# Kernel optimization log

Measured on AMD Instinct MI355X. Metric: run time of the kernel, lower is better.

## Reference

```python
import jax, jax.numpy as jnp
import numpy as np

N = 50000      # nodes
E = 800000     # edges
D_IN = 256     # state_dim
H = 128        # HIDDEN_LAYER
A = 32         # action_dim
EPS = 1e-5
NEG_SLOPE = 0.2


def setup_inputs() -> dict:
    key = jax.random.key(0)
    ks = jax.random.split(key, 16)
    s = lambda k, shape, std=0.1: jax.random.normal(k, shape, jnp.float32) * std
    return {
        "x": jax.random.normal(ks[0], (N, D_IN), jnp.float32),
        "edge_index": jax.random.randint(ks[1], (2, E), 0, N, jnp.int64),
        # GAT params
        "W": s(ks[2], (D_IN, H)),
        "a_src": s(ks[3], (H,)),
        "a_dst": s(ks[4], (H,)),
        "b_gat": jnp.zeros((H,), jnp.float32),
        # bn0
        "g0": jnp.ones((H,), jnp.float32),
        "beta0": jnp.zeros((H,), jnp.float32),
        # fc1, fc2
        "W1": s(ks[5], (H, H)),
        "b1": jnp.zeros((H,), jnp.float32),
        "W2": s(ks[6], (H, H)),
        "b2": jnp.zeros((H,), jnp.float32),
        # bn2
        "g2": jnp.ones((H,), jnp.float32),
        "beta2": jnp.zeros((H,), jnp.float32),
        # fc3
        "W3": s(ks[7], (H, A)),
        "b3": jnp.zeros((A,), jnp.float32),
    }


def _batchnorm(h, gamma, beta):
    # training-mode BN: biased batch stats over node dim
    mu = jnp.mean(h, axis=0)
    var = jnp.var(h, axis=0)
    return (h - mu) * jax.lax.rsqrt(var + EPS) * gamma + beta


def _gat(x, edge_index, W, a_src, a_dst, b_gat):
    src, dst = edge_index[0], edge_index[1]
    h = x @ W                                  # [N, H]
    e_src = h @ a_src                          # [N]
    e_dst = h @ a_dst                          # [N]
    e = jax.nn.leaky_relu(e_src[src] + e_dst[dst], NEG_SLOPE)  # [E]
    # neighbor softmax over edges grouped by destination node
    m = jax.ops.segment_max(e, dst, num_segments=N)            # [N]
    w = jnp.exp(e - m[dst])                                    # [E]
    denom = jax.ops.segment_sum(w, dst, num_segments=N)        # [N]
    alpha = w / jnp.maximum(denom, 1e-16)[dst]                 # [E]
    out = jax.ops.segment_sum(alpha[:, None] * h[src], dst, num_segments=N)
    return out + b_gat


def reference(x, edge_index, W, a_src, a_dst, b_gat, g0, beta0,
              W1, b1, W2, b2, g2, beta2, W3, b3):
    h0 = jax.nn.relu(_gat(x, edge_index, W, a_src, a_dst, b_gat))
    h0n = _batchnorm(h0, g0, beta0)
    h1 = jax.nn.relu(h0n @ W1 + b1)
    h2 = jax.nn.relu(h1 @ W2 + b2)
    h2n = _batchnorm(h2, g2, beta2)
    action = h2n @ W3 + b3
    return jax.nn.softmax(action, axis=1)
```

## Files before the change

kernel.cpp:

```cpp
#include <hip/hip_runtime.h>
#include <math.h>

#define N_NODES 50000
#define N_EDGES 800000
#define D_INPUT 256
#define HDIM 128
#define A_DIM 32
#define NEG_SLOPE 0.2f
#define BN_EPS 1e-5f
#define CAP 64
#define NB 391
#define BIN_SHIFT 7
#define BCAP 2432
#define GC_STRIDE 16
#define EPB 4096
#define FC3_TR 64
#define SROW 132

typedef short short8 __attribute__((ext_vector_type(8)));
typedef unsigned short ushort8v __attribute__((ext_vector_type(8)));
typedef unsigned short ushort4v __attribute__((ext_vector_type(4)));
typedef float float4v __attribute__((ext_vector_type(4)));

__device__ __forceinline__ unsigned short f2bf(float f) {
  unsigned u = __float_as_uint(f);
  u += 0x7FFFu + ((u >> 16) & 1u);
  return (unsigned short)(u >> 16);
}
__device__ __forceinline__ float bf2f(unsigned short b) {
  return __uint_as_float(((unsigned)b) << 16);
}

__device__ __forceinline__ float waveReduceMax(float v) {
#pragma unroll
  for (int o = 32; o >= 1; o >>= 1) v = fmaxf(v, __shfl_xor(v, o, 64));
  return v;
}
__device__ __forceinline__ float waveReduceSum(float v) {
#pragma unroll
  for (int o = 32; o >= 1; o >>= 1) v += __shfl_xor(v, o, 64);
  return v;
}

__global__ __launch_bounds__(256) void k_gemm_xw_mfma(
    const float* __restrict__ x, const unsigned short* __restrict__ Wt0,
    const float* __restrict__ a_src, const float* __restrict__ a_dst,
    unsigned short* __restrict__ hbf, float* __restrict__ esrc, float* __restrict__ edst)
{
  __shared__ short As[64][72];
  __shared__ short Bs[128][72];
  __shared__ float esred[64][2], edred[64][2];

  const int t = threadIdx.x;
  const int lane = t & 63;
  const int wv = t >> 6;
  const int rh = wv >> 1;
  const int ch = wv & 1;
  const int quad = (lane >> 4) & 3;
  const int l15 = lane & 15;
  const int row0 = blockIdx.x * 64;

  float4v acc[2][4];
#pragma unroll
  for (int i = 0; i < 2; ++i)
#pragma unroll
    for (int j = 0; j < 4; ++j) acc[i][j] = (float4v){0.f, 0.f, 0.f, 0.f};

  for (int ks = 0; ks < D_INPUT / 64; ++ks) {
    const int kk0 = ks * 64;
#pragma unroll
    for (int it = 0; it < 4; ++it) {
      int idx = it * 256 + t;
      int r = idx >> 4, c4 = idx & 15;
      int rr = row0 + r; if (rr >= N_NODES) rr = N_NODES - 1;
      float4 v = *(const float4*)(x + (size_t)rr * D_INPUT + kk0 + c4 * 4);
      ushort4v b; b.x = f2bf(v.x); b.y = f2bf(v.y); b.z = f2bf(v.z); b.w = f2bf(v.w);
      *(ushort4v*)(&As[r][c4 * 4]) = b;
    }
#pragma unroll
    for (int it = 0; it < 4; ++it) {
      int idx = it * 256 + t;
      int n = idx >> 3, c8 = idx & 7;
      *(ushort8v*)(&Bs[n][c8 * 8]) = *(const ushort8v*)(Wt0 + (size_t)n * D_INPUT + kk0 + c8 * 8);
    }
    __syncthreads();
#pragma unroll
    for (int kc = 0; kc < 2; ++kc) {
      short8 af[2], bfr[4];
#pragma unroll
      for (int rt = 0; rt < 2; ++rt)
        af[rt] = *(const short8*)(&As[rh * 32 + rt * 16 + l15][kc * 32 + quad * 8]);
#pragma unroll
      for (int nt = 0; nt < 4; ++nt)
        bfr[nt] = *(const short8*)(&Bs[ch * 64 + nt * 16 + l15][kc * 32 + quad * 8]);
#pragma unroll
      for (int rt = 0; rt < 2; ++rt)
#pragma unroll
        for (int nt = 0; nt < 4; ++nt)
          acc[rt][nt] = __builtin_amdgcn_mfma_f32_16x16x32_bf16(af[rt], bfr[nt], acc[rt][nt], 0, 0, 0);
    }
    __syncthreads();
  }

  float asv[4], adv[4];
#pragma unroll
  for (int nt = 0; nt < 4; ++nt) {
    int col = ch * 64 + nt * 16 + l15;
    asv[nt] = a_src[col]; adv[nt] = a_dst[col];
  }
#pragma unroll
  for (int rt = 0; rt < 2; ++rt) {
#pragma unroll
    for (int reg = 0; reg < 4; ++reg) {
      int rloc = rh * 32 + rt * 16 + quad * 4 + reg;
      int row = row0 + rloc;
      bool valid = (row < N_NODES);
      float ps = 0.f, pd = 0.f;
#pragma unroll
      for (int nt = 0; nt < 4; ++nt) {
        float v = acc[rt][nt][reg];
        ps += v * asv[nt]; pd += v * adv[nt];
        if (valid) hbf[(size_t)row * HDIM + ch * 64 + nt * 16 + l15] = f2bf(v);
      }
#pragma unroll
      for (int o = 8; o >= 1; o >>= 1) {
        ps += __shfl_xor(ps, o, 64);
        pd += __shfl_xor(pd, o, 64);
      }
      if (l15 == 0) { esred[rloc][ch] = ps; edred[rloc][ch] = pd; }
    }
  }
  __syncthreads();
  if (t < 64) {
    int row = row0 + t;
    if (row < N_NODES) {
      esrc[row] = esred[t][0] + esred[t][1];
      edst[row] = edred[t][0] + edred[t][1];
    }
  }
}

__global__ __launch_bounds__(256) void k_binprep(
    const int* __restrict__ srcI, const int* __restrict__ dstI,
    int* __restrict__ gcur, int* __restrict__ bbuf,
    const float* __restrict__ W, const float* __restrict__ W1,
    const float* __restrict__ W2, unsigned short* __restrict__ Wt0,
    unsigned short* __restrict__ Wt1, unsigned short* __restrict__ Wt2)
{
  const int gB = (N_EDGES + EPB - 1) / EPB;
  if (blockIdx.x >= gB) {
    int i = (blockIdx.x - gB) * 256 + threadIdx.x;
    if (i < HDIM * D_INPUT) {
      int n = i >> 8, k = i & 255;
      Wt0[i] = f2bf(W[(size_t)k * HDIM + n]);
    }
    if (i < HDIM * HDIM) {
      int n = i >> 7, k = i & 127;
      Wt1[i] = f2bf(W1[(size_t)k * HDIM + n]);
      Wt2[i] = f2bf(W2[(size_t)k * HDIM + n]);
    }
    return;
  }
  __shared__ int hist[NB];
  __shared__ int base[NB];
  const int t = threadIdx.x;
  const int e0 = blockIdx.x * EPB;
  const int e1 = min(e0 + EPB, N_EDGES);
  for (int i = t; i < NB; i += 256) hist[i] = 0;
  __syncthreads();
  for (int e = e0 + t; e < e1; e += 256)
    atomicAdd(&hist[dstI[e] >> BIN_SHIFT], 1);
  __syncthreads();
  for (int i = t; i < NB; i += 256) {
    base[i] = atomicAdd(&gcur[i * GC_STRIDE], hist[i]);
    hist[i] = 0;
  }
  __syncthreads();
  for (int e = e0 + t; e < e1; e += 256) {
    int d = dstI[e];
    int bin = d >> BIN_SHIFT;
    int r = atomicAdd(&hist[bin], 1) + base[bin];
    if (r < BCAP) bbuf[(size_t)bin * BCAP + r] = srcI[e] | ((d & 127) << 16);
  }
}

__global__ __launch_bounds__(256) void k_sc2(
    const int* __restrict__ gcur, const int* __restrict__ bbuf,
    const float* __restrict__ esrc, const float* __restrict__ edst,
    int* __restrict__ deg, int2* __restrict__ sedge)
{
  __shared__ int2 bk[128][CAP];
  __shared__ int lcur[128];
  __shared__ float ledst[128];
  const int t = threadIdx.x;
  const int bin = blockIdx.x;
  const int d0 = bin << BIN_SHIFT;
  if (t < 128) {
    lcur[t] = 0;
    int d = d0 + t;
    ledst[t] = (d < N_NODES) ? edst[d] : 0.f;
  }
  __syncthreads();
  const int cnt = min(gcur[bin * GC_STRIDE], BCAP);
  const int* seg = bbuf + (size_t)bin * BCAP;
  for (int i = t; i < cnt; i += 256) {
    int v = seg[i];
    int s = v & 0xFFFF;
    int dl = (v >> 16) & 127;
    float ev = esrc[s] + ledst[dl];
    ev = (ev > 0.f) ? ev : NEG_SLOPE * ev;
    int r = atomicAdd(&lcur[dl], 1);
    if (r < CAP) {
      int2 e2; e2.x = s; e2.y = __float_as_int(ev);
      bk[dl][r] = e2;
    }
  }
  __syncthreads();
  for (int idx = t; idx < 128 * CAP; idx += 256) {
    int dl = idx >> 6, sl = idx & 63;
    if (sl < lcur[dl])
      sedge[(size_t)(d0 + dl) * CAP + sl] = bk[dl][sl];
  }
  if (t < 128) {
    int d = d0 + t;
    if (d < N_NODES) deg[d] = min(lcur[t], CAP);
  }
}

__global__ __launch_bounds__(256) void k_agg(
    const int* __restrict__ degA, const int2* __restrict__ sedge,
    const unsigned short* __restrict__ hbf,
    const float* __restrict__ b_gat, unsigned short* __restrict__ h0)
{
  const int t = threadIdx.x;
  const int lane = t & 63;
  const int node = blockIdx.x * 4 + (t >> 6);
  const int deg = min(degA[node], CAP);

  int2 ev; ev.x = 0; ev.y = 0;
  float val = -INFINITY;
  if (lane < deg) {
    ev = sedge[(size_t)node * CAP + lane];
    val = __int_as_float(ev.y);
  }
  const float m = waveReduceMax(val);
  const float ex = (lane < deg) ? __expf(val - m) : 0.f;
  const float s = waveReduceSum(ex);
  const float al = ex * (1.0f / fmaxf(s, 1e-16f));
  const int sr = ev.x;

  float ax = 0.f, ay = 0.f;
  int j = 0;
  for (; j + 4 <= deg; j += 4) {
    float a0 = __shfl(al, j, 64),   a1 = __shfl(al, j+1, 64);
    float a2 = __shfl(al, j+2, 64), a3 = __shfl(al, j+3, 64);
    int s0 = __shfl(sr, j, 64),   s1 = __shfl(sr, j+1, 64);
    int s2 = __shfl(sr, j+2, 64), s3 = __shfl(sr, j+3, 64);
    unsigned v0 = *(const unsigned*)(hbf + (size_t)s0 * HDIM + lane * 2);
    unsigned v1 = *(const unsigned*)(hbf + (size_t)s1 * HDIM + lane * 2);
    unsigned v2 = *(const unsigned*)(hbf + (size_t)s2 * HDIM + lane * 2);
    unsigned v3 = *(const unsigned*)(hbf + (size_t)s3 * HDIM + lane * 2);
    ax += a0 * bf2f((unsigned short)(v0 & 0xFFFFu))
        + a1 * bf2f((unsigned short)(v1 & 0xFFFFu))
        + a2 * bf2f((unsigned short)(v2 & 0xFFFFu))
        + a3 * bf2f((unsigned short)(v3 & 0xFFFFu));
    ay += a0 * bf2f((unsigned short)(v0 >> 16))
        + a1 * bf2f((unsigned short)(v1 >> 16))
        + a2 * bf2f((unsigned short)(v2 >> 16))
        + a3 * bf2f((unsigned short)(v3 >> 16));
  }
  for (; j < deg; ++j) {
    float a = __shfl(al, j, 64);
    int sj = __shfl(sr, j, 64);
    unsigned v = *(const unsigned*)(hbf + (size_t)sj * HDIM + lane * 2);
    ax += a * bf2f((unsigned short)(v & 0xFFFFu));
    ay += a * bf2f((unsigned short)(v >> 16));
  }
  float vx = fmaxf(ax + b_gat[lane * 2], 0.f);
  float vy = fmaxf(ay + b_gat[lane * 2 + 1], 0.f);
  *(unsigned*)(h0 + (size_t)node * HDIM + lane * 2) =
      (unsigned)f2bf(vx) | ((unsigned)f2bf(vy) << 16);
}

#define BN_ROWS 256
__global__ __launch_bounds__(256) void k_bnstats(
    const unsigned short* __restrict__ src, float* __restrict__ gsum, float* __restrict__ gsq)
{
  __shared__ float red[16][128];
  const int t = threadIdx.x;
  const int cg = t & 15;
  const int rl = t >> 4;
  const int row0 = blockIdx.x * BN_ROWS;
  float s[8], q[8];
#pragma unroll
  for (int j = 0; j < 8; ++j) { s[j] = 0.f; q[j] = 0.f; }
  for (int i = 0; i < BN_ROWS / 16; ++i) {
    int row = row0 + rl + i * 16;
    if (row < N_NODES) {
      ushort8v v = *(const ushort8v*)(src + (size_t)row * HDIM + cg * 8);
#pragma unroll
      for (int j = 0; j < 8; ++j) {
        float f = bf2f(v[j]);
        s[j] += f; q[j] += f * f;
      }
    }
  }
#pragma unroll
  for (int j = 0; j < 8; ++j) red[rl][cg * 8 + j] = s[j];
  __syncthreads();
  if (t < 128) {
    float S = 0.f;
#pragma unroll
    for (int r = 0; r < 16; ++r) S += red[r][t];
    atomicAdd(&gsum[t], S);
  }
  __syncthreads();
#pragma unroll
  for (int j = 0; j < 8; ++j) red[rl][cg * 8 + j] = q[j];
  __syncthreads();
  if (t < 128) {
    float Q = 0.f;
#pragma unroll
    for (int r = 0; r < 16; ++r) Q += red[r][t];
    atomicAdd(&gsq[t], Q);
  }
}

__global__ __launch_bounds__(256) void k_fc12(
    const unsigned short* __restrict__ in,
    const float* __restrict__ gsumIn, const float* __restrict__ gsqIn,
    const float* __restrict__ gamma, const float* __restrict__ beta,
    const unsigned short* __restrict__ Wt1, const float* __restrict__ b1,
    const unsigned short* __restrict__ Wt2, const float* __restrict__ b2,
    unsigned short* __restrict__ outp,
    float* __restrict__ gsum, float* __restrict__ gsq)
{
  __shared__ short As[64 * SROW];
  __shared__ short Bsh[128 * SROW];
  __shared__ float statS[128][2], statQ[128][2];
  __shared__ float sc[HDIM], shf[HDIM];

  const int t = threadIdx.x;
  const int lane = t & 63;
  const int wv = t >> 6;
  const int rh = wv >> 1;
  const int ch = wv & 1;
  const int quad = (lane >> 4) & 3;
  const int l15 = lane & 15;
  const int row0 = blockIdx.x * 64;

  if (t < HDIM) {
    float mean = gsumIn[t] / (float)N_NODES;
    float var = gsqIn[t] / (float)N_NODES - mean * mean;
    float s = gamma[t] * rsqrtf(var + BN_EPS);
    sc[t] = s; shf[t] = beta[t] - mean * s;
  }
  __syncthreads();

#pragma unroll
  for (int it = 0; it < 4; ++it) {
    int idx = it * 256 + t;
    int r = idx >> 4, c8 = idx & 15;
    int rr = row0 + r; if (rr >= N_NODES) rr = N_NODES - 1;
    ushort8v v = *(const ushort8v*)(in + (size_t)rr * HDIM + c8 * 8);
#pragma unroll
    for (int j = 0; j < 8; ++j) {
      int k = c8 * 8 + j;
      v[j] = f2bf(bf2f(v[j]) * sc[k] + shf[k]);
    }
    *(ushort8v*)(&As[r * SROW + c8 * 8]) = v;
  }
#pragma unroll
  for (int it = 0; it < 8; ++it) {
    int idx = it * 256 + t;
    int n = idx >> 4, c8 = idx & 15;
    *(ushort8v*)(&Bsh[n * SROW + c8 * 8]) = *(const ushort8v*)(Wt1 + (size_t)n * HDIM + c8 * 8);
  }
  __syncthreads();

  float4v acc[2][4];
#pragma unroll
  for (int i = 0; i < 2; ++i)
#pragma unroll
    for (int j = 0; j < 4; ++j) acc[i][j] = (float4v){0.f, 0.f, 0.f, 0.f};

#pragma unroll
  for (int kc = 0; kc < 4; ++kc) {
    short8 af[2], bfr[4];
#pragma unroll
    for (int rt = 0; rt < 2; ++rt)
      af[rt] = *(const short8*)(&As[(rh * 32 + rt * 16 + l15) * SROW + kc * 32 + quad * 8]);
#pragma unroll
    for (int nt = 0; nt < 4; ++nt)
      bfr[nt] = *(const short8*)(&Bsh[(ch * 64 + nt * 16 + l15) * SROW + kc * 32 + quad * 8]);
#pragma unroll
    for (int rt = 0; rt < 2; ++rt)
#pragma unroll
      for (int nt = 0; nt < 4; ++nt)
        acc[rt][nt] = __builtin_amdgcn_mfma_f32_16x16x32_bf16(af[rt], bfr[nt], acc[rt][nt], 0, 0, 0);
  }
  __syncthreads();

  {
    float bv[4];
#pragma unroll
    for (int nt = 0; nt < 4; ++nt) bv[nt] = b1[ch * 64 + nt * 16 + l15];
#pragma unroll
    for (int rt = 0; rt < 2; ++rt) {
#pragma unroll
      for (int reg = 0; reg < 4; ++reg) {
        int rloc = rh * 32 + rt * 16 + quad * 4 + reg;
#pragma unroll
        for (int nt = 0; nt < 4; ++nt) {
          float o = fmaxf(acc[rt][nt][reg] + bv[nt], 0.f);
          As[rloc * SROW + ch * 64 + nt * 16 + l15] = f2bf(o);
        }
      }
    }
  }
#pragma unroll
  for (int it = 0; it < 8; ++it) {
    int idx = it * 256 + t;
    int n = idx >> 4, c8 = idx & 15;
    *(ushort8v*)(&Bsh[n * SROW + c8 * 8]) = *(const ushort8v*)(Wt2 + (size_t)n * HDIM + c8 * 8);
  }
  __syncthreads();

#pragma unroll
  for (int i = 0; i < 2; ++i)
#pragma unroll
    for (int j = 0; j < 4; ++j) acc[i][j] = (float4v){0.f, 0.f, 0.f, 0.f};

#pragma unroll
  for (int kc = 0; kc < 4; ++kc) {
    short8 af[2], bfr[4];
#pragma unroll
    for (int rt = 0; rt < 2; ++rt)
      af[rt] = *(const short8*)(&As[(rh * 32 + rt * 16 + l15) * SROW + kc * 32 + quad * 8]);
#pragma unroll
    for (int nt = 0; nt < 4; ++nt)
      bfr[nt] = *(const short8*)(&Bsh[(ch * 64 + nt * 16 + l15) * SROW + kc * 32 + quad * 8]);
#pragma unroll
    for (int rt = 0; rt < 2; ++rt)
#pragma unroll
      for (int nt = 0; nt < 4; ++nt)
        acc[rt][nt] = __builtin_amdgcn_mfma_f32_16x16x32_bf16(af[rt], bfr[nt], acc[rt][nt], 0, 0, 0);
  }

  float bv[4];
#pragma unroll
  for (int nt = 0; nt < 4; ++nt) bv[nt] = b2[ch * 64 + nt * 16 + l15];

  float pS[4] = {0.f, 0.f, 0.f, 0.f}, pQ[4] = {0.f, 0.f, 0.f, 0.f};
#pragma unroll
  for (int rt = 0; rt < 2; ++rt) {
#pragma unroll
    for (int reg = 0; reg < 4; ++reg) {
      int row = row0 + rh * 32 + rt * 16 + quad * 4 + reg;
      bool valid = (row < N_NODES);
#pragma unroll
      for (int nt = 0; nt < 4; ++nt) {
        float o = fmaxf(acc[rt][nt][reg] + bv[nt], 0.f);
        if (valid) {
          outp[(size_t)row * HDIM + ch * 64 + nt * 16 + l15] = f2bf(o);
          pS[nt] += o; pQ[nt] += o * o;
        }
      }
    }
  }
#pragma unroll
  for (int nt = 0; nt < 4; ++nt) {
    float s = pS[nt], q = pQ[nt];
    s += __shfl_xor(s, 16, 64); s += __shfl_xor(s, 32, 64);
    q += __shfl_xor(q, 16, 64); q += __shfl_xor(q, 32, 64);
    if (lane < 16) {
      statS[ch * 64 + nt * 16 + lane][rh] = s;
      statQ[ch * 64 + nt * 16 + lane][rh] = q;
    }
  }
  __syncthreads();
  if (t < 128) {
    atomicAdd(&gsum[t], statS[t][0] + statS[t][1]);
    atomicAdd(&gsq[t],  statQ[t][0] + statQ[t][1]);
  }
}

__global__ __launch_bounds__(128) void k_fc3(
    const unsigned short* __restrict__ h2,
    const float* __restrict__ gsumIn, const float* __restrict__ gsqIn,
    const float* __restrict__ gamma, const float* __restrict__ beta,
    const float* __restrict__ W3, const float* __restrict__ b3,
    float* __restrict__ out)
{
  __shared__ float w3p[HDIM][A_DIM];
  __shared__ float hs[HDIM][FC3_TR + 2];
  __shared__ float s2s[HDIM], sh2s[HDIM];
  __shared__ float bred[4][A_DIM];
  __shared__ float b3p[A_DIM];
  const int t = threadIdx.x;

  {
    float mean = gsumIn[t] / (float)N_NODES;
    float var = gsqIn[t] / (float)N_NODES - mean * mean;
    float s = gamma[t] * rsqrtf(var + BN_EPS);
    s2s[t] = s; sh2s[t] = beta[t] - mean * s;
  }
  __syncthreads();

  for (int i = t; i < HDIM * A_DIM; i += 128) {
    int k = i >> 5;
    w3p[k][i & 31] = s2s[k] * W3[i];
  }
  {
    int j = t & 31, seg = t >> 5;
    float p = 0.f;
    for (int kk = 0; kk < 32; ++kk) {
      int k = seg * 32 + kk;
      p += sh2s[k] * W3[k * A_DIM + j];
    }
    bred[seg][j] = p;
  }
  const int row0 = blockIdx.x * FC3_TR;
  for (int i = t; i < FC3_TR * (HDIM / 8); i += 128) {
    int r = i & 63, cg = i >> 6;
    int row = row0 + r;
    ushort8v v;
    if (row < N_NODES) v = *(const ushort8v*)(h2 + (size_t)row * HDIM + cg * 8);
    else { for (int jj = 0; jj < 8; ++jj) v[jj] = 0; }
#pragma unroll
    for (int jj = 0; jj < 8; ++jj) hs[cg * 8 + jj][r] = bf2f(v[jj]);
  }
  __syncthreads();
  if (t < 32) b3p[t] = b3[t] + bred[0][t] + bred[1][t] + bred[2][t] + bred[3][t];
  __syncthreads();

  const int r0 = (t >> 3) * 4;
  const int j0 = (t & 7) * 4;
  float4 acc[4];
#pragma unroll
  for (int r = 0; r < 4; ++r) acc[r] = (float4){0.f, 0.f, 0.f, 0.f};

  for (int k = 0; k < HDIM; k += 4) {
    float4 w0 = *(const float4*)&w3p[k + 0][j0];
    float4 w1 = *(const float4*)&w3p[k + 1][j0];
    float4 w2 = *(const float4*)&w3p[k + 2][j0];
    float4 w3v = *(const float4*)&w3p[k + 3][j0];
#pragma unroll
    for (int r = 0; r < 4; ++r) {
      int rr = r0 + r;
      float h0 = hs[k + 0][rr], h1 = hs[k + 1][rr];
      float h2v = hs[k + 2][rr], h3 = hs[k + 3][rr];
      acc[r].x += h0 * w0.x + h1 * w1.x + h2v * w2.x + h3 * w3v.x;
      acc[r].y += h0 * w0.y + h1 * w1.y + h2v * w2.y + h3 * w3v.y;
      acc[r].z += h0 * w0.z + h1 * w1.z + h2v * w2.z + h3 * w3v.z;
      acc[r].w += h0 * w0.w + h1 * w1.w + h2v * w2.w + h3 * w3v.w;
    }
  }

  float4 b4 = *(const float4*)&b3p[j0];
#pragma unroll
  for (int r = 0; r < 4; ++r) {
    float l0 = acc[r].x + b4.x, l1 = acc[r].y + b4.y;
    float l2 = acc[r].z + b4.z, l3 = acc[r].w + b4.w;
    float mx = fmaxf(fmaxf(l0, l1), fmaxf(l2, l3));
#pragma unroll
    for (int o = 1; o <= 4; o <<= 1) mx = fmaxf(mx, __shfl_xor(mx, o, 64));
    float e0 = __expf(l0 - mx), e1 = __expf(l1 - mx);
    float e2 = __expf(l2 - mx), e3 = __expf(l3 - mx);
    float sm = e0 + e1 + e2 + e3;
#pragma unroll
    for (int o = 1; o <= 4; o <<= 1) sm += __shfl_xor(sm, o, 64);
    float inv = 1.0f / sm;
    int row = row0 + r0 + r;
    if (row < N_NODES) {
      float4 o4; o4.x = e0 * inv; o4.y = e1 * inv; o4.z = e2 * inv; o4.w = e3 * inv;
      *(float4*)(out + (size_t)row * A_DIM + j0) = o4;
    }
  }
}

extern "C" void kernel_launch(void* const* d_in, const int* in_sizes, int n_in,
                              void* d_out, int out_size, void* d_ws, size_t ws_size,
                              hipStream_t stream) {
  const float* x     = (const float*)d_in[0];
  const int*   ei    = (const int*)d_in[1];
  const float* W     = (const float*)d_in[2];
  const float* a_src = (const float*)d_in[3];
  const float* a_dst = (const float*)d_in[4];
  const float* b_gat = (const float*)d_in[5];
  const float* g0    = (const float*)d_in[6];
  const float* beta0 = (const float*)d_in[7];
  const float* W1    = (const float*)d_in[8];
  const float* b1    = (const float*)d_in[9];
  const float* W2    = (const float*)d_in[10];
  const float* b2    = (const float*)d_in[11];
  const float* g2    = (const float*)d_in[12];
  const float* beta2 = (const float*)d_in[13];
  const float* W3    = (const float*)d_in[14];
  const float* b3    = (const float*)d_in[15];
  float* out = (float*)d_out;
  const int* srcI = ei;
  const int* dstI = ei + N_EDGES;

  char* p = (char*)d_ws;
  auto alloc = [&](size_t bytes) -> char* {
    char* q = p; p += (bytes + 255) & ~(size_t)255; return q;
  };
  unsigned short* h   = (unsigned short*)alloc(sizeof(short) * (size_t)N_NODES * HDIM);
  unsigned short* h0  = (unsigned short*)alloc(sizeof(short) * (size_t)N_NODES * HDIM);
  unsigned short* h2  = h;
  unsigned short* Wt0 = (unsigned short*)alloc(sizeof(short) * HDIM * D_INPUT);
  unsigned short* Wt1 = (unsigned short*)alloc(sizeof(short) * HDIM * HDIM);
  unsigned short* Wt2 = (unsigned short*)alloc(sizeof(short) * HDIM * HDIM);
  int2*  sedge  = (int2*)alloc(sizeof(int2) * (size_t)N_NODES * CAP);
  int*   bbuf   = (int*)alloc(sizeof(int) * (size_t)NB * BCAP);
  float* esrc   = (float*)alloc(sizeof(float) * N_NODES);
  float* edst   = (float*)alloc(sizeof(float) * N_NODES);
  int*   deg    = (int*)alloc(sizeof(int) * N_NODES);
  char*  zbase  = alloc(sizeof(int) * NB * GC_STRIDE + 256 + sizeof(float) * 4 * 128);
  int*   gcur   = (int*)zbase;
  float* stats  = (float*)(zbase + ((sizeof(int) * NB * GC_STRIDE + 255) & ~(size_t)255));
  float* gsum0 = stats;        float* gsq0  = stats + 128;
  float* gsum2 = stats + 256;  float* gsq2  = stats + 384;
  size_t zsize = (size_t)((char*)(stats + 512) - zbase);

  hipMemsetAsync(zbase, 0, zsize, stream);

  const int gT = (N_NODES + 63) / 64;
  const int gB = (N_EDGES + EPB - 1) / EPB;
  const int gP = (HDIM * D_INPUT + 255) / 256;

  k_binprep<<<gB + gP, 256, 0, stream>>>(srcI, dstI, gcur, bbuf,
                                         W, W1, W2, Wt0, Wt1, Wt2);
  k_gemm_xw_mfma<<<gT, 256, 0, stream>>>(x, Wt0, a_src, a_dst, h, esrc, edst);
  k_sc2<<<NB, 256, 0, stream>>>(gcur, bbuf, esrc, edst, deg, sedge);
  k_agg<<<N_NODES / 4, 256, 0, stream>>>(deg, sedge, h, b_gat, h0);
  k_bnstats<<<(N_NODES + BN_ROWS - 1) / BN_ROWS, 256, 0, stream>>>(h0, gsum0, gsq0);
  k_fc12<<<gT, 256, 0, stream>>>(h0, gsum0, gsq0, g0, beta0, Wt1, b1, Wt2, b2, h2,
                                 gsum2, gsq2);
  k_fc3<<<(N_NODES + FC3_TR - 1) / FC3_TR, 128, 0, stream>>>(
      h2, gsum2, gsq2, g2, beta2, W3, b3, out);
}
```

Before: 265.0 us.

## Merge edge binning into the X·W GEMM kernel and replace memset with prep kernel

Weight transposition/bf16 conversion and zeroing of the bin counters and BN stats move into a small prep kernel, which replaces the hipMemsetAsync. Edge binning now runs as extra blocks of the GEMM launch, so the memory-bound binning can overlap with the compute-bound X·W matmul. This removes one launch and one memset and lets the two independent workloads share the GPU at once. The cost is that the GEMM blocks now reserve the hist/base shared arrays as well, which may lower occupancy.

```diff
diff --git a/kernel.cpp b/kernel.cpp
--- a/kernel.cpp
+++ b/kernel.cpp
@@ -42,16 +42,64 @@
   return v;
 }
 
-__global__ __launch_bounds__(256) void k_gemm_xw_mfma(
+__global__ __launch_bounds__(256) void k_prep(
+    const float* __restrict__ W, const float* __restrict__ W1,
+    const float* __restrict__ W2, unsigned short* __restrict__ Wt0,
+    unsigned short* __restrict__ Wt1, unsigned short* __restrict__ Wt2,
+    int* __restrict__ gcur, float* __restrict__ stats)
+{
+  int i = blockIdx.x * 256 + threadIdx.x;
+  if (i < HDIM * D_INPUT) {
+    int n = i >> 8, k = i & 255;
+    Wt0[i] = f2bf(W[(size_t)k * HDIM + n]);
+  }
+  if (i < HDIM * HDIM) {
+    int n = i >> 7, k = i & 127;
+    Wt1[i] = f2bf(W1[(size_t)k * HDIM + n]);
+    Wt2[i] = f2bf(W2[(size_t)k * HDIM + n]);
+  }
+  if (i < NB * GC_STRIDE) gcur[i] = 0;
+  if (i < 512) stats[i] = 0.f;
+}
+
+__global__ __launch_bounds__(256) void k_gemmbin(
     const float* __restrict__ x, const unsigned short* __restrict__ Wt0,
     const float* __restrict__ a_src, const float* __restrict__ a_dst,
-    unsigned short* __restrict__ hbf, float* __restrict__ esrc, float* __restrict__ edst)
+    unsigned short* __restrict__ hbf, float* __restrict__ esrc, float* __restrict__ edst,
+    const int* __restrict__ srcI, const int* __restrict__ dstI,
+    int* __restrict__ gcur, int* __restrict__ bbuf)
 {
+  const int gT = (N_NODES + 63) / 64;
   __shared__ short As[64][72];
   __shared__ short Bs[128][72];
   __shared__ float esred[64][2], edred[64][2];
+  __shared__ int hist[NB];
+  __shared__ int base[NB];
 
   const int t = threadIdx.x;
+
+  if (blockIdx.x >= gT) {
+    const int e0 = (blockIdx.x - gT) * EPB;
+    const int e1 = min(e0 + EPB, N_EDGES);
+    for (int i = t; i < NB; i += 256) hist[i] = 0;
+    __syncthreads();
+    for (int e = e0 + t; e < e1; e += 256)
+      atomicAdd(&hist[dstI[e] >> BIN_SHIFT], 1);
+    __syncthreads();
+    for (int i = t; i < NB; i += 256) {
+      base[i] = atomicAdd(&gcur[i * GC_STRIDE], hist[i]);
+      hist[i] = 0;
+    }
+    __syncthreads();
+    for (int e = e0 + t; e < e1; e += 256) {
+      int d = dstI[e];
+      int bin = d >> BIN_SHIFT;
+      int r = atomicAdd(&hist[bin], 1) + base[bin];
+      if (r < BCAP) bbuf[(size_t)bin * BCAP + r] = srcI[e] | ((d & 127) << 16);
+    }
+    return;
+  }
+
   const int lane = t & 63;
   const int wv = t >> 6;
   const int rh = wv >> 1;
@@ -137,50 +185,6 @@
       esrc[row] = esred[t][0] + esred[t][1];
       edst[row] = edred[t][0] + edred[t][1];
     }
-  }
-}
-
-__global__ __launch_bounds__(256) void k_binprep(
-    const int* __restrict__ srcI, const int* __restrict__ dstI,
-    int* __restrict__ gcur, int* __restrict__ bbuf,
-    const float* __restrict__ W, const float* __restrict__ W1,
-    const float* __restrict__ W2, unsigned short* __restrict__ Wt0,
-    unsigned short* __restrict__ Wt1, unsigned short* __restrict__ Wt2)
-{
-  const int gB = (N_EDGES + EPB - 1) / EPB;
-  if (blockIdx.x >= gB) {
-    int i = (blockIdx.x - gB) * 256 + threadIdx.x;
-    if (i < HDIM * D_INPUT) {
-      int n = i >> 8, k = i & 255;
-      Wt0[i] = f2bf(W[(size_t)k * HDIM + n]);
-    }
-    if (i < HDIM * HDIM) {
-      int n = i >> 7, k = i & 127;
-      Wt1[i] = f2bf(W1[(size_t)k * HDIM + n]);
-      Wt2[i] = f2bf(W2[(size_t)k * HDIM + n]);
-    }
-    return;
-  }
-  __shared__ int hist[NB];
-  __shared__ int base[NB];
-  const int t = threadIdx.x;
-  const int e0 = blockIdx.x * EPB;
-  const int e1 = min(e0 + EPB, N_EDGES);
-  for (int i = t; i < NB; i += 256) hist[i] = 0;
-  __syncthreads();
-  for (int e = e0 + t; e < e1; e += 256)
-    atomicAdd(&hist[dstI[e] >> BIN_SHIFT], 1);
-  __syncthreads();
-  for (int i = t; i < NB; i += 256) {
-    base[i] = atomicAdd(&gcur[i * GC_STRIDE], hist[i]);
-    hist[i] = 0;
-  }
-  __syncthreads();
-  for (int e = e0 + t; e < e1; e += 256) {
-    int d = dstI[e];
-    int bin = d >> BIN_SHIFT;
-    int r = atomicAdd(&hist[bin], 1) + base[bin];
-    if (r < BCAP) bbuf[(size_t)bin * BCAP + r] = srcI[e] | ((d & 127) << 16);
   }
 }
 
@@ -617,22 +621,18 @@
   float* esrc   = (float*)alloc(sizeof(float) * N_NODES);
   float* edst   = (float*)alloc(sizeof(float) * N_NODES);
   int*   deg    = (int*)alloc(sizeof(int) * N_NODES);
-  char*  zbase  = alloc(sizeof(int) * NB * GC_STRIDE + 256 + sizeof(float) * 4 * 128);
-  int*   gcur   = (int*)zbase;
-  float* stats  = (float*)(zbase + ((sizeof(int) * NB * GC_STRIDE + 255) & ~(size_t)255));
+  int*   gcur   = (int*)alloc(sizeof(int) * NB * GC_STRIDE);
+  float* stats  = (float*)alloc(sizeof(float) * 4 * 128);
   float* gsum0 = stats;        float* gsq0  = stats + 128;
   float* gsum2 = stats + 256;  float* gsq2  = stats + 384;
-  size_t zsize = (size_t)((char*)(stats + 512) - zbase);
-
-  hipMemsetAsync(zbase, 0, zsize, stream);
 
   const int gT = (N_NODES + 63) / 64;
   const int gB = (N_EDGES + EPB - 1) / EPB;
   const int gP = (HDIM * D_INPUT + 255) / 256;
 
-  k_binprep<<<gB + gP, 256, 0, stream>>>(srcI, dstI, gcur, bbuf,
-                                         W, W1, W2, Wt0, Wt1, Wt2);
-  k_gemm_xw_mfma<<<gT, 256, 0, stream>>>(x, Wt0, a_src, a_dst, h, esrc, edst);
+  k_prep<<<gP, 256, 0, stream>>>(W, W1, W2, Wt0, Wt1, Wt2, gcur, stats);
+  k_gemmbin<<<gT + gB, 256, 0, stream>>>(x, Wt0, a_src, a_dst, h, esrc, edst,
+                                         srcI, dstI, gcur, bbuf);
   k_sc2<<<NB, 256, 0, stream>>>(gcur, bbuf, esrc, edst, deg, sedge);
   k_agg<<<N_NODES / 4, 256, 0, stream>>>(deg, sedge, h, b_gat, h0);
   k_bnstats<<<(N_NODES + BN_ROWS - 1) / BN_ROWS, 256, 0, stream>>>(h0, gsum0, gsq0);
```

Measured after the change: 248.4 us. 1.07x faster.
